# Kernel tuning notes

Hardware: AMD Instinct MI355X
Metric: run time of the kernel (lower is better)

## Reference

```python
import jax, jax.numpy as jnp
import numpy as np
from jax import lax

DG = 16          # deformable_groups
K = 9            # 3x3 kernel taps
PAD = 1
MAX_RES = 10.0   # max_residue_magnitude


def conv3x3(x, w, b):
    # NCHW / OIHW, stride 1, SAME padding (pad=1 for 3x3)
    return lax.conv_general_dilated(x, w, (1, 1), 'SAME',
                                    dimension_numbers=('NCHW', 'OIHW', 'NCHW')) + b[None, :, None, None]


def lrelu(x):
    return jnp.where(x >= 0, x, 0.1 * x)


def setup_inputs() -> dict:
    key = jax.random.key(0)
    ks = jax.random.split(key, 10)
    B, C, H, W = 4, 64, 128, 128
    Cout = 64
    coff_in = 2 * C + 2          # (1 + pa_frames//2)*C + pa_frames, pa_frames=2
    nch = 3 * K * DG             # 432 offset/mask channels

    def mkw(k, o, i, scale=1.0):
        return jax.random.normal(k, (o, i, 3, 3), jnp.float32) * (scale / np.sqrt(i * 9))

    return {
        'x': jax.random.normal(ks[0], (B, C, H, W), jnp.float32),
        'x_flow_warped': jax.random.normal(ks[1], (B, C, H, W), jnp.float32),
        'x_current': jax.random.normal(ks[2], (B, C, H, W), jnp.float32),
        'flow': jax.random.normal(ks[3], (B, 2, H, W), jnp.float32) * 2.0,
        'w1': mkw(ks[4], Cout, coff_in), 'b1': jnp.zeros((Cout,), jnp.float32),
        'w2': mkw(ks[5], Cout, Cout),    'b2': jnp.zeros((Cout,), jnp.float32),
        'w3': mkw(ks[6], Cout, Cout),    'b3': jnp.zeros((Cout,), jnp.float32),
        'w4': mkw(ks[7], nch, Cout, 0.1), 'b4': jnp.zeros((nch,), jnp.float32),
        'weight': mkw(ks[8], Cout, C),   'bias': jnp.zeros((Cout,), jnp.float32),
    }


def deform_conv2d(x, offset, mask, weight, bias):
    # modulated deformable conv, 3x3, stride 1, pad 1, dilation 1, groups=1
    B, C, H, W = x.shape
    O = weight.shape[0]
    dg, Cg = DG, C // DG
    off = offset.reshape(B, dg, K, 2, H, W)
    dy, dx = off[:, :, :, 0], off[:, :, :, 1]        # (B,dg,K,H,W), (y,x) pairs
    ki = jnp.arange(3)
    ii, jj = jnp.meshgrid(ki, ki, indexing='ij')
    ii = ii.reshape(K).astype(jnp.float32)
    jj = jj.reshape(K).astype(jnp.float32)
    # sampling coords in input space: h - pad + i + dy, w - pad + j + dx
    py = dy + (jnp.arange(H, dtype=jnp.float32) - PAD)[None, None, None, :, None] + ii[None, None, :, None, None]
    px = dx + (jnp.arange(W, dtype=jnp.float32) - PAD)[None, None, None, None, :] + jj[None, None, :, None, None]
    y0 = jnp.floor(py)
    x0 = jnp.floor(px)
    wy1 = py - y0
    wx1 = px - x0
    y0i = y0.astype(jnp.int32)
    x0i = x0.astype(jnp.int32)
    xg = x.reshape(B, dg, Cg, H * W)

    def gather(yi, xi):
        valid = ((yi >= 0) & (yi < H) & (xi >= 0) & (xi < W)).astype(x.dtype)  # zero outside
        idx = (jnp.clip(yi, 0, H - 1) * W + jnp.clip(xi, 0, W - 1)).reshape(B, dg, 1, K * H * W)
        v = jnp.take_along_axis(xg, jnp.broadcast_to(idx, (B, dg, Cg, K * H * W)), axis=-1)
        return v.reshape(B, dg, Cg, K, H, W) * valid[:, :, None]

    s = (gather(y0i, x0i)         * ((1 - wy1) * (1 - wx1))[:, :, None]
         + gather(y0i, x0i + 1)   * ((1 - wy1) * wx1)[:, :, None]
         + gather(y0i + 1, x0i)   * (wy1 * (1 - wx1))[:, :, None]
         + gather(y0i + 1, x0i + 1) * (wy1 * wx1)[:, :, None])
    s = s * mask.reshape(B, dg, 1, K, H, W)
    s = s.reshape(B, C, K, H, W)
    return jnp.einsum('bckhw,ock->bohw', s, weight.reshape(O, C, K)) + bias[None, :, None, None]


def reference(x, x_flow_warped, x_current, flow, w1, b1, w2, b2, w3, b3, w4, b4, weight, bias):
    feat = jnp.concatenate([x_flow_warped, x_current, flow], axis=1)
    h = lrelu(conv3x3(feat, w1, b1))
    h = lrelu(conv3x3(h, w2, b2))
    h = lrelu(conv3x3(h, w3, b3))
    out = conv3x3(h, w4, b4)
    o1, o2, mask = jnp.split(out, 3, axis=1)
    offset = MAX_RES * jnp.tanh(jnp.concatenate([o1, o2], axis=1))
    flowf = flow[:, ::-1]  # flip (x,y) -> (y,x)
    offset = offset + jnp.tile(flowf, (1, offset.shape[1] // 2, 1, 1))
    mask = jax.nn.sigmoid(mask)
    return deform_conv2d(x, offset, mask, weight, bias)
```

## Files before the change

kernel.cpp:

```cpp
#include <hip/hip_runtime.h>
#include <math.h>
#include <type_traits>

#define BH 4
#define HH 128
#define WW 128
#define HW (HH * WW)
#define SSTR 600

typedef __attribute__((ext_vector_type(8))) short bf16x8;
typedef __attribute__((ext_vector_type(4))) float f32x4;
typedef unsigned uint4a __attribute__((ext_vector_type(4), aligned(4)));

__device__ inline short f2bf(float f) {
    union { float f; unsigned u; } x; x.f = f;
    unsigned r = x.u + 0x7fff + ((x.u >> 16) & 1);
    return (short)(r >> 16);
}
__device__ inline float bf2f(short h) {
    union { unsigned u; float f; } x; x.u = ((unsigned)(unsigned short)h) << 16;
    return x.f;
}
__device__ inline float bflo(unsigned u) {
    union { unsigned u; float f; } x; x.u = u << 16; return x.f;
}
__device__ inline float bfhi(unsigned u) {
    union { unsigned u; float f; } x; x.u = u & 0xffff0000u; return x.f;
}

struct RepackArgs {
    const float* w[5];
    short* dst[5];
    int off[6];
};

__device__ inline void repack_generic(const float* w, short* dst, int g,
                                      int M, int Cin, int T, int MT)
{
    int lane = g & 63;
    int f = g >> 6;
    int mt = f % MT;
    int kt = f / MT;
    int tap = kt % T;
    int kc = kt / T;
    int m = mt * 16 + (lane & 15);
    int ic0 = kc * 32 + (lane >> 4) * 8;
    short v[8];
#pragma unroll
    for (int i = 0; i < 8; ++i) {
        int ic = ic0 + i;
        float x = (m < M && ic < Cin) ? w[((size_t)m * Cin + ic) * T + tap] : 0.f;
        v[i] = f2bf(x);
    }
    *(bf16x8*)(dst + (size_t)g * 8) = *(const bf16x8*)v;
}

__global__ __launch_bounds__(256) void repack_all_k(RepackArgs a)
{
    int g = blockIdx.x * 256 + threadIdx.x;
    if (g < a.off[1]) {
        repack_generic(a.w[0], a.dst[0], g - a.off[0], 64, 130, 9, 4);
    } else if (g < a.off[2]) {
        repack_generic(a.w[1], a.dst[1], g - a.off[1], 64, 64, 9, 4);
    } else if (g < a.off[3]) {
        repack_generic(a.w[2], a.dst[2], g - a.off[2], 64, 64, 9, 4);
    } else if (g < a.off[4]) {
        repack_generic(a.w[3], a.dst[3], g - a.off[3], 432, 64, 9, 27);
    } else if (g < a.off[5]) {
        int gg = g - a.off[4];
        int lane = gg & 63;
        int f = gg >> 6;
        int mt = f & 3, kc = f >> 2;
        int m = mt * 16 + (lane & 15);
        int ck0 = kc * 32 + (lane >> 4) * 8;
        short v[8];
#pragma unroll
        for (int i = 0; i < 8; ++i) {
            int ck = ck0 + i;
            int dg = ck / 36, rem = ck % 36;
            int k = rem >> 2, cg = rem & 3;
            int c = dg * 4 + cg;
            v[i] = f2bf(a.w[4][((size_t)m * 64 + c) * 9 + k]);
        }
        *(bf16x8*)(a.dst[4] + (size_t)gg * 8) = *(const bf16x8*)v;
    }
}

__global__ __launch_bounds__(256) void prep_k(
    const float* __restrict__ xfw, const float* __restrict__ xcur,
    const float* __restrict__ flow, const float* __restrict__ x,
    short* __restrict__ cc, short* __restrict__ xt)
{
    int tid = threadIdx.x;
    int z = blockIdx.z;
    int px = blockIdx.x * 256 + tid;
    if (z < BH) {
        int b = z;
        const float* s0 = xfw + (size_t)b * 64 * HW + px;
        const float* s1 = xcur + (size_t)b * 64 * HW + px;
        const float* s2 = flow + (size_t)b * 2 * HW + px;
        short v[144];
#pragma unroll
        for (int c = 0; c < 64; ++c) v[c] = f2bf(s0[(size_t)c * HW]);
#pragma unroll
        for (int c = 0; c < 64; ++c) v[64 + c] = f2bf(s1[(size_t)c * HW]);
        v[128] = f2bf(s2[0]);
        v[129] = f2bf(s2[HW]);
#pragma unroll
        for (int c = 130; c < 144; ++c) v[c] = 0;
        short* dst = cc + ((size_t)b * HW + px) * 144;
#pragma unroll
        for (int q = 0; q < 18; ++q)
            *(bf16x8*)(dst + q * 8) = *(const bf16x8*)&v[q * 8];
    } else {
        int b = z - BH;
        const float* src = x + (size_t)b * 64 * HW + px;
        short v[64];
#pragma unroll
        for (int c = 0; c < 64; ++c) v[c] = f2bf(src[(size_t)c * HW]);
        short* dstb = xt + (size_t)b * 16 * HW * 4 + (size_t)px * 4;
#pragma unroll
        for (int d = 0; d < 16; ++d)
            *(uint2*)(dstb + (size_t)d * HW * 4) = *(const uint2*)&v[d * 4];
    }
}

template<int CSTR, int KC, bool ACT, int MTW>
__global__ __launch_bounds__(256) void conv_mfma_k(
    const short* __restrict__ in, const short* __restrict__ wp,
    const float* __restrict__ bias, short* __restrict__ out,
    int Cout, int MB, int MT)
{
    __shared__ alignas(16) short X[3 * 66 * 40];
    const int tid = threadIdx.x;
    const int lane = tid & 63, wv = tid >> 6;
    const int x0 = blockIdx.x * 64, y = blockIdx.y;
    const int zb = blockIdx.z;
    const int b = zb / MB, mb = zb % MB;

    int mtg[MTW];
#pragma unroll
    for (int mt = 0; mt < MTW; ++mt) {
        int t = (mb * 4 + wv) * MTW + mt;
        mtg[mt] = (t < MT) ? t : MT - 1;
    }

    const int r = tid / 66, c = tid - r * 66;
    const int yy = y + r - 1, xx = x0 + c - 1;
    const bool inb = (tid < 198) && (yy >= 0 && yy < HH && xx >= 0 && xx < WW);
    const short* srcp = in + ((size_t)b * HW + (size_t)yy * WW + xx) * CSTR;
    short* dstp = &X[(r * 66 + c) * 40];

    f32x4 acc[MTW][4] = {};

    for (int kc = 0; kc < KC; ++kc) {
        __syncthreads();
        if (tid < 198) {
            if (inb) {
                const short* s0 = srcp + kc * 32;
#pragma unroll
                for (int g = 0; g < 4; ++g)
                    *(bf16x8*)&dstp[g * 8] = *(const bf16x8*)&s0[g * 8];
            } else {
                bf16x8 z = {};
#pragma unroll
                for (int g = 0; g < 4; ++g) *(bf16x8*)&dstp[g * 8] = z;
            }
        }
        __syncthreads();
#pragma unroll
        for (int tap = 0; tap < 9; ++tap) {
            const int dy = tap / 3, dx = tap - dy * 3;
            bf16x8 a[MTW];
#pragma unroll
            for (int mt = 0; mt < MTW; ++mt)
                a[mt] = *(const bf16x8*)(wp + (((size_t)(kc * 9 + tap) * MT + mtg[mt]) * 64 + lane) * 8);
#pragma unroll
            for (int nt = 0; nt < 4; ++nt) {
                int cc2 = nt * 16 + (lane & 15) + dx;
                bf16x8 bb = *(const bf16x8*)&X[(dy * 66 + cc2) * 40 + (lane >> 4) * 8];
#pragma unroll
                for (int mt = 0; mt < MTW; ++mt)
                    acc[mt][nt] = __builtin_amdgcn_mfma_f32_16x16x32_bf16(a[mt], bb, acc[mt][nt], 0, 0, 0);
            }
        }
    }

    const int xl = lane & 15, rg = lane >> 4;
#pragma unroll
    for (int mt = 0; mt < MTW; ++mt) {
        int t = (mb * 4 + wv) * MTW + mt;
        int m0 = t * 16;
        if (m0 >= Cout) continue;
#pragma unroll
        for (int nt = 0; nt < 4; ++nt) {
            int xx2 = x0 + nt * 16 + xl;
            short pk[4];
#pragma unroll
            for (int j = 0; j < 4; ++j) {
                int o = m0 + rg * 4 + j;
                float rv = acc[mt][nt][j] + bias[o];
                if (ACT) rv = (rv >= 0.f) ? rv : 0.1f * rv;
                pk[j] = f2bf(rv);
            }
            *(uint2*)(out + ((size_t)b * HW + (size_t)y * WW + xx2) * (size_t)Cout
                      + m0 + rg * 4) = *(const uint2*)pk;
        }
    }
}

__global__ __launch_bounds__(256) void dcn_k(
    const short* __restrict__ xt, const float* __restrict__ flow,
    const short* __restrict__ out4, const short* __restrict__ wtp,
    const float* __restrict__ bias, float* __restrict__ out)
{
    __shared__ alignas(16) short s[16 * SSTR];
    const int tid = threadIdx.x;
    const int b = blockIdx.z, y = blockIdx.y, xb = blockIdx.x * 16;
    const size_t hw = (size_t)HW;
    constexpr float L2E = 1.4426950408889634f;

    const int lane = tid & 63, wv = tid >> 6;
    const int p = tid & 15;
    const int dg = tid >> 4;
    const int xp = xb + p;
    const size_t pix = (size_t)y * WW + xp;
    const short* xg = xt + ((size_t)b * 16 + dg) * hw * 4;
    const short* o4p = out4 + ((size_t)b * hw + pix) * 432;
    const float fl0 = flow[((size_t)b * 2 + 0) * hw + pix];
    const float fl1 = flow[((size_t)b * 2 + 1) * hw + pix];

    const unsigned* pd = (const unsigned*)o4p + 9 * dg;
    const short* pm = o4p + 288 + 9 * dg;
    short* sp = &s[p * SSTR + dg * 36];

#pragma unroll
    for (int it = 0; it < 9; ++it) {
        unsigned dyx = pd[it];
        float omk = bf2f(pm[it]);
        float ody = bflo(dyx), odx = bfhi(dyx);
        float tdy = 1.f - 2.f * __builtin_amdgcn_rcpf(__builtin_amdgcn_exp2f(2.f * L2E * ody) + 1.f);
        float tdx = 1.f - 2.f * __builtin_amdgcn_rcpf(__builtin_amdgcn_exp2f(2.f * L2E * odx) + 1.f);
        float m   = __builtin_amdgcn_rcpf(1.f + __builtin_amdgcn_exp2f(-L2E * omk));

        float py = 10.f * tdy + fl1 + (float)(y  - 1 + it / 3);
        float px = 10.f * tdx + fl0 + (float)(xp - 1 + it % 3);
        float fy = floorf(py), fx = floorf(px);
        int iy0 = (int)fy, ix0 = (int)fx;
        float wy1 = py - fy, wx1 = px - fx;
        float wy0 = 1.f - wy1, wx0 = 1.f - wx1;
        int iy1 = iy0 + 1, ix1 = ix0 + 1;
        bool vy0 = (iy0 >= 0) & (iy0 < HH), vy1 = (iy1 >= 0) & (iy1 < HH);
        bool vx0 = (ix0 >= 0) & (ix0 < WW), vx1 = (ix1 >= 0) & (ix1 < WW);
        float w00 = (vy0 & vx0) ? wy0 * wx0 : 0.f;
        float w01 = (vy0 & vx1) ? wy0 * wx1 : 0.f;
        float w10 = (vy1 & vx0) ? wy1 * wx0 : 0.f;
        float w11 = (vy1 & vx1) ? wy1 * wx1 : 0.f;
        int cy0 = min(max(iy0, 0), HH - 1), cy1 = min(max(iy1, 0), HH - 1);

        int bx = min(max(ix0, 0), WW - 2);
        int cx0 = min(max(ix0, 0), WW - 1);
        int cx1 = min(max(ix0 + 1, 0), WW - 1);
        bool s0 = (cx0 != bx);
        bool s1 = (cx1 != bx);
        uint4a r0 = *(const uint4a*)(xg + (size_t)(cy0 * WW + bx) * 4);
        uint4a r1 = *(const uint4a*)(xg + (size_t)(cy1 * WW + bx) * 4);
        unsigned d00x = s0 ? r0.z : r0.x, d00y = s0 ? r0.w : r0.y;
        unsigned d01x = s1 ? r0.z : r0.x, d01y = s1 ? r0.w : r0.y;
        unsigned d10x = s0 ? r1.z : r1.x, d10y = s0 ? r1.w : r1.y;
        unsigned d11x = s1 ? r1.z : r1.x, d11y = s1 ? r1.w : r1.y;

        float a0 = w00 * bflo(d00x) + w01 * bflo(d01x) + w10 * bflo(d10x) + w11 * bflo(d11x);
        float a1 = w00 * bfhi(d00x) + w01 * bfhi(d01x) + w10 * bfhi(d10x) + w11 * bfhi(d11x);
        float a2 = w00 * bflo(d00y) + w01 * bflo(d01y) + w10 * bflo(d10y) + w11 * bflo(d11y);
        float a3 = w00 * bfhi(d00y) + w01 * bfhi(d01y) + w10 * bfhi(d10y) + w11 * bfhi(d11y);

        uint2 t;
        t.x = ((unsigned)(unsigned short)f2bf(a1 * m) << 16) | (unsigned short)f2bf(a0 * m);
        t.y = ((unsigned)(unsigned short)f2bf(a3 * m) << 16) | (unsigned short)f2bf(a2 * m);
        *(uint2*)&sp[it * 4] = t;
    }
    __syncthreads();

    f32x4 acc = {};
#pragma unroll
    for (int kc = 0; kc < 18; ++kc) {
        bf16x8 a = *(const bf16x8*)(wtp + ((size_t)(kc * 4 + wv) * 64 + lane) * 8);
        bf16x8 bb = *(const bf16x8*)&s[(lane & 15) * SSTR + kc * 32 + (lane >> 4) * 8];
        acc = __builtin_amdgcn_mfma_f32_16x16x32_bf16(a, bb, acc, 0, 0, 0);
    }

    const int xl = lane & 15, rg = lane >> 4;
#pragma unroll
    for (int j = 0; j < 4; ++j) {
        int o = wv * 16 + rg * 4 + j;
        out[((size_t)(b * 64 + o) * HH + y) * WW + xb + xl] = acc[j] + bias[o];
    }
}

extern "C" void kernel_launch(void* const* d_in, const int* in_sizes, int n_in,
                              void* d_out, int out_size, void* d_ws, size_t ws_size,
                              hipStream_t stream)
{
    const float* x    = (const float*)d_in[0];
    const float* xfw  = (const float*)d_in[1];
    const float* xcur = (const float*)d_in[2];
    const float* flow = (const float*)d_in[3];
    const float* w1   = (const float*)d_in[4];
    const float* b1   = (const float*)d_in[5];
    const float* w2   = (const float*)d_in[6];
    const float* b2   = (const float*)d_in[7];
    const float* w3   = (const float*)d_in[8];
    const float* b3   = (const float*)d_in[9];
    const float* w4   = (const float*)d_in[10];
    const float* b4   = (const float*)d_in[11];
    const float* wt   = (const float*)d_in[12];
    const float* bs   = (const float*)d_in[13];

    const size_t hw = (size_t)HW;
    short* out4 = (short*)d_ws;
    short* h1   = out4 + (size_t)BH * hw * 432;
    short* h2   = h1 + (size_t)BH * hw * 64;
    short* cc   = h2 + (size_t)BH * hw * 64;
    short* xt   = cc + (size_t)BH * hw * 144 + 256;
    short* wp1  = xt + (size_t)BH * hw * 64 + 256;
    short* wp2  = wp1 + (size_t)180 * 512;
    short* wp3  = wp2 + (size_t)72 * 512;
    short* wp4  = wp3 + (size_t)72 * 512;
    short* wtp  = wp4 + (size_t)486 * 512;

    RepackArgs ra;
    ra.w[0] = w1; ra.w[1] = w2; ra.w[2] = w3; ra.w[3] = w4; ra.w[4] = wt;
    ra.dst[0] = wp1; ra.dst[1] = wp2; ra.dst[2] = wp3; ra.dst[3] = wp4; ra.dst[4] = wtp;
    int tot[5] = {11520, 4608, 4608, 31104, 4608};
    ra.off[0] = 0;
    for (int i = 0; i < 5; ++i) ra.off[i + 1] = ra.off[i] + tot[i];
    repack_all_k<<<(ra.off[5] + 255) / 256, 256, 0, stream>>>(ra);

    prep_k<<<dim3(HW / 256, 1, 2 * BH), 256, 0, stream>>>(xfw, xcur, flow, x, cc, xt);

    dim3 blk(256);
    conv_mfma_k<144, 5, true,  1><<<dim3(2, 128, BH),     blk, 0, stream>>>(cc, wp1, b1, h1, 64, 1, 4);
    conv_mfma_k<64,  2, true,  1><<<dim3(2, 128, BH),     blk, 0, stream>>>(h1, wp2, b2, h2, 64, 1, 4);
    conv_mfma_k<64,  2, true,  1><<<dim3(2, 128, BH),     blk, 0, stream>>>(h2, wp3, b3, h1, 64, 1, 4);
    conv_mfma_k<64,  2, false, 4><<<dim3(2, 128, BH * 2), blk, 0, stream>>>(h1, wp4, b4, out4, 432, 2, 27);

    dcn_k<<<dim3(WW / 16, HH, BH), blk, 0, stream>>>(xt, flow, out4, wtp, bs, (float*)d_out);
}
```

Baseline: 193.9 us.

## Store offset/mask conv output in 16-pixel-block channel-major layout for coalesced DCN reads

The last offset conv now writes its output in a blocked layout. For each 16-pixel record, channels are outermost and the 16 pixels are contiguous, with offset pairs packed as 32-bit words and masks kept in a separate array. The deformable-conv kernel then reads each tap's offset and mask with lanes p striding contiguously instead of at a 432-element stride per pixel, which should coalesce its loads. In exchange, the conv epilogue does scattered 4-byte and 2-byte stores instead of 8-byte vector stores, which may cost write efficiency.

```diff
diff --git a/kernel.cpp b/kernel.cpp
--- a/kernel.cpp
+++ b/kernel.cpp
@@ -125,10 +125,11 @@
     }
 }
 
-template<int CSTR, int KC, bool ACT, int MTW>
+template<int CSTR, int KC, bool ACT, int MTW, bool QMAJ>
 __global__ __launch_bounds__(256) void conv_mfma_k(
     const short* __restrict__ in, const short* __restrict__ wp,
     const float* __restrict__ bias, short* __restrict__ out,
+    unsigned* __restrict__ outp, short* __restrict__ outm,
     int Cout, int MB, int MT)
 {
     __shared__ alignas(16) short X[3 * 66 * 40];
@@ -203,16 +204,34 @@
                 if (ACT) rv = (rv >= 0.f) ? rv : 0.1f * rv;
                 pk[j] = f2bf(rv);
             }
-            *(uint2*)(out + ((size_t)b * HW + (size_t)y * WW + xx2) * (size_t)Cout
-                      + m0 + rg * 4) = *(const uint2*)pk;
+            if (QMAJ) {
+                int blk = (y * WW + xx2) >> 4;
+                size_t rec = (size_t)b * (HW / 16) + blk;
+                if (t < 18) {
+                    int q0 = (m0 + rg * 4) >> 1;
+                    unsigned d0 = ((unsigned)(unsigned short)pk[1] << 16) | (unsigned short)pk[0];
+                    unsigned d1 = ((unsigned)(unsigned short)pk[3] << 16) | (unsigned short)pk[2];
+                    outp[(rec * 144 + q0) * 16 + xl]     = d0;
+                    outp[(rec * 144 + q0 + 1) * 16 + xl] = d1;
+                } else {
+                    int c0 = m0 + rg * 4 - 288;
+#pragma unroll
+                    for (int j = 0; j < 4; ++j)
+                        outm[(rec * 144 + c0 + j) * 16 + xl] = pk[j];
+                }
+            } else {
+                *(uint2*)(out + ((size_t)b * HW + (size_t)y * WW + xx2) * (size_t)Cout
+                          + m0 + rg * 4) = *(const uint2*)pk;
+            }
         }
     }
 }
 
 __global__ __launch_bounds__(256) void dcn_k(
     const short* __restrict__ xt, const float* __restrict__ flow,
-    const short* __restrict__ out4, const short* __restrict__ wtp,
-    const float* __restrict__ bias, float* __restrict__ out)
+    const unsigned* __restrict__ o4p, const short* __restrict__ o4m,
+    const short* __restrict__ wtp, const float* __restrict__ bias,
+    float* __restrict__ out)
 {
     __shared__ alignas(16) short s[16 * SSTR];
     const int tid = threadIdx.x;
@@ -226,18 +245,18 @@
     const int xp = xb + p;
     const size_t pix = (size_t)y * WW + xp;
     const short* xg = xt + ((size_t)b * 16 + dg) * hw * 4;
-    const short* o4p = out4 + ((size_t)b * hw + pix) * 432;
     const float fl0 = flow[((size_t)b * 2 + 0) * hw + pix];
     const float fl1 = flow[((size_t)b * 2 + 1) * hw + pix];
 
-    const unsigned* pd = (const unsigned*)o4p + 9 * dg;
-    const short* pm = o4p + 288 + 9 * dg;
+    const size_t rec = (size_t)b * (HW / 16) + ((size_t)y * 8 + blockIdx.x);
+    const unsigned* pd = o4p + (rec * 144 + 9 * dg) * 16 + p;
+    const short* pm = o4m + (rec * 144 + 9 * dg) * 16 + p;
     short* sp = &s[p * SSTR + dg * 36];
 
 #pragma unroll
     for (int it = 0; it < 9; ++it) {
-        unsigned dyx = pd[it];
-        float omk = bf2f(pm[it]);
+        unsigned dyx = pd[it * 16];
+        float omk = bf2f(pm[it * 16]);
         float ody = bflo(dyx), odx = bfhi(dyx);
         float tdy = 1.f - 2.f * __builtin_amdgcn_rcpf(__builtin_amdgcn_exp2f(2.f * L2E * ody) + 1.f);
         float tdx = 1.f - 2.f * __builtin_amdgcn_rcpf(__builtin_amdgcn_exp2f(2.f * L2E * odx) + 1.f);
@@ -318,8 +337,9 @@
     const float* bs   = (const float*)d_in[13];
 
     const size_t hw = (size_t)HW;
-    short* out4 = (short*)d_ws;
-    short* h1   = out4 + (size_t)BH * hw * 432;
+    unsigned* o4p = (unsigned*)d_ws;
+    short*    o4m = (short*)(o4p + (size_t)BH * (hw / 16) * 144 * 16);
+    short* h1   = (short*)d_ws + (size_t)BH * hw * 432;
     short* h2   = h1 + (size_t)BH * hw * 64;
     short* cc   = h2 + (size_t)BH * hw * 64;
     short* xt   = cc + (size_t)BH * hw * 144 + 256;
@@ -340,10 +360,14 @@
     prep_k<<<dim3(HW / 256, 1, 2 * BH), 256, 0, stream>>>(xfw, xcur, flow, x, cc, xt);
 
     dim3 blk(256);
-    conv_mfma_k<144, 5, true,  1><<<dim3(2, 128, BH),     blk, 0, stream>>>(cc, wp1, b1, h1, 64, 1, 4);
-    conv_mfma_k<64,  2, true,  1><<<dim3(2, 128, BH),     blk, 0, stream>>>(h1, wp2, b2, h2, 64, 1, 4);
-    conv_mfma_k<64,  2, true,  1><<<dim3(2, 128, BH),     blk, 0, stream>>>(h2, wp3, b3, h1, 64, 1, 4);
-    conv_mfma_k<64,  2, false, 4><<<dim3(2, 128, BH * 2), blk, 0, stream>>>(h1, wp4, b4, out4, 432, 2, 27);
-
-    dcn_k<<<dim3(WW / 16, HH, BH), blk, 0, stream>>>(xt, flow, out4, wtp, bs, (float*)d_out);
-}
+    conv_mfma_k<144, 5, true,  1, false><<<dim3(2, 128, BH),     blk, 0, stream>>>(
+        cc, wp1, b1, h1, nullptr, nullptr, 64, 1, 4);
+    conv_mfma_k<64,  2, true,  1, false><<<dim3(2, 128, BH),     blk, 0, stream>>>(
+        h1, wp2, b2, h2, nullptr, nullptr, 64, 1, 4);
+    conv_mfma_k<64,  2, true,  1, false><<<dim3(2, 128, BH),     blk, 0, stream>>>(
+        h2, wp3, b3, h1, nullptr, nullptr, 64, 1, 4);
+    conv_mfma_k<64,  2, false, 4, true ><<<dim3(2, 128, BH * 2), blk, 0, stream>>>(
+        h1, wp4, b4, nullptr, o4p, o4m, 432, 2, 27);
+
+    dcn_k<<<dim3(WW / 16, HH, BH), blk, 0, stream>>>(xt, flow, o4p, o4m, wtp, bs, (float*)d_out);
+}
```

After: 193.4 us. No clear change (-0.3%).
